# Kernel optimization log

Measured on AMD Instinct MI355X. Metric: run time of the kernel, lower is better.

The kernel has to match this reference:

```python
import jax, jax.numpy as jnp
import numpy as np

B, T, D, H = 4, 2048, 1024, 16
HD = D // H  # head_dim = 64


def setup_inputs() -> dict:
    key = jax.random.key(0)
    ks = jax.random.split(key, 7)
    x = jax.random.normal(ks[0], (B, T, D), dtype=jnp.float32)
    engagement = jax.random.uniform(ks[1], (B, T), dtype=jnp.float32)
    mask = jax.random.uniform(ks[2], (B, T)) < 0.1  # True = masked-out key
    s = 1.0 / np.sqrt(D)
    qkv_w = jax.random.normal(ks[3], (3 * D, D), dtype=jnp.float32) * s
    qkv_b = jax.random.normal(ks[4], (3 * D,), dtype=jnp.float32) * 0.02
    out_w = jax.random.normal(ks[5], (D, D), dtype=jnp.float32) * s
    out_b = jax.random.normal(ks[6], (D,), dtype=jnp.float32) * 0.02
    return {"x": x, "engagement": engagement, "mask": mask,
            "qkv_w": qkv_w, "qkv_b": qkv_b, "out_w": out_w, "out_b": out_b}


def reference(x, engagement, mask, qkv_w, qkv_b, out_w, out_b):
    b, t, d = x.shape
    qkv = x @ qkv_w.T + qkv_b                       # [B,T,3D]
    q, k, v = jnp.split(qkv, 3, axis=-1)
    # [B,T,D] -> [B,H,T,HD]
    to_heads = lambda a: a.reshape(b, t, H, HD).transpose(0, 2, 1, 3)
    q, k, v = to_heads(q), to_heads(k), to_heads(v)
    attn = jnp.einsum('bhqd,bhkd->bhqk', q, k) / jnp.sqrt(jnp.float32(HD))
    log_g = jnp.log(jnp.clip(engagement, 1e-6))     # [B,T] per-key bias
    attn = attn + log_g[:, None, None, :]
    attn = jnp.where(mask[:, None, None, :], jnp.float32(-1e9), attn)
    p = jax.nn.softmax(attn, axis=-1)
    o = jnp.einsum('bhqk,bhkd->bhqd', p, v)         # [B,H,T,HD]
    o = o.transpose(0, 2, 1, 3).reshape(b, t, d)    # [B,T,D]
    return o @ out_w.T + out_b
```

## Files before the change

### kernel.cpp

```cpp
#include <hip/hip_runtime.h>
#include <math.h>

#define B_  4
#define T_  2048
#define D_  1024
#define H_  16
#define HD_ 64

typedef unsigned short ushort_t;
typedef unsigned int uint_t;
typedef __attribute__((ext_vector_type(8))) short bf16x8;
typedef __attribute__((ext_vector_type(4))) float f32x4;

#define SC_LOG2 0.1803368801111243f

__device__ inline ushort_t f2bf(float f) {
  uint_t u = __float_as_uint(f);
  u += 0x7fffu + ((u >> 16) & 1u);
  return (ushort_t)(u >> 16);
}
__device__ inline ushort_t f2bf_fast(float f) {
  return (ushort_t)((__float_as_uint(f) + 0x8000u) >> 16);
}
__device__ inline uint_t cvtpk_bf16(float lo, float hi) {
  uint_t r;
  asm("v_cvt_pk_bf16_f32 %0, %1, %2" : "=v"(r) : "v"(lo), "v"(hi));
  return r;
}

__device__ inline void gload_lds16(const ushort_t* g, ushort_t* l) {
  __builtin_amdgcn_global_load_lds(
      (const __attribute__((address_space(1))) unsigned int*)g,
      (__attribute__((address_space(3))) unsigned int*)l, 16, 0, 0);
}

__global__ __launch_bounds__(256) void cvt_bf16(const float* __restrict__ in,
                                                ushort_t* __restrict__ out, int n) {
  int i = (blockIdx.x * 256 + threadIdx.x) * 4;
  if (i + 3 < n) {
    float4 v = *(const float4*)(in + i);
    uint_t lo = (uint_t)f2bf(v.x) | ((uint_t)f2bf(v.y) << 16);
    uint_t hi = (uint_t)f2bf(v.z) | ((uint_t)f2bf(v.w) << 16);
    *(uint2*)(out + i) = make_uint2(lo, hi);
  }
}

__global__ __launch_bounds__(256) void bias_prep(const float* __restrict__ eng,
                                                 const int* __restrict__ mask,
                                                 float* __restrict__ biasA, int n) {
  int i = blockIdx.x * 256 + threadIdx.x;
  if (i < n) biasA[i] = mask[i] ? -1e30f : __log2f(fmaxf(eng[i], 1e-6f));
}

#define CHUNKS_ 32

#define STAGE_CHUNK(CK, SLOT)                                                  \
  {                                                                            \
    const int ck_ = (CK);                                                      \
    ushort_t* sb_ = lds + (SLOT) * SLOT_E;                                     \
    gload_lds16(Ag + (size_t)ck_ * 32, sb_ + w * 512);                         \
    if constexpr (BN == 256) {                                                 \
      gload_lds16(Bg + (size_t)ck_ * 32, sb_ + 4096 + w * 1024);               \
      gload_lds16(Bg + 16384 + (size_t)ck_ * 32, sb_ + 4096 + w * 1024 + 512); \
    } else {                                                                   \
      gload_lds16(Bg + (size_t)ck_ * 32, sb_ + 4096 + w * 512);                \
    }                                                                          \
  }

template <int WRITE_BF16, int BN>
__global__ __launch_bounds__(512, 4) void gemm256(
    const ushort_t* __restrict__ A, const ushort_t* __restrict__ Bm,
    const float* __restrict__ bias, void* __restrict__ Cout,
    int N, int nbx) {
  constexpr int SLOT_E = 4096 + BN * 32;
  constexpr int NBB = BN / 64;
  constexpr int WCOLS = BN / 4;
  __shared__ __align__(16) ushort_t lds[3 * SLOT_E];

  const int tid = threadIdx.x;
  const int w = tid >> 6, lane = tid & 63;
  const int l15 = lane & 15, quad = lane >> 4;
  const int wr = w >> 2, wc = w & 3;

  int wg = blockIdx.x;
  const int cpx = gridDim.x >> 3;
  wg = (wg & 7) * cpx + (wg >> 3);
  const int m0 = (wg / nbx) * 128, n0 = (wg % nbx) * BN;

  const int gc = (lane & 3) ^ ((lane >> 3) & 3);
  const ushort_t* Ag = A + (size_t)(m0 + w * 16 + (lane >> 2)) * 1024 + gc * 8;
  const ushort_t* Bg =
      Bm + (size_t)(n0 + w * (BN / 8) + (lane >> 2)) * 1024 + gc * 8;

  const int p8 = (quad ^ ((l15 >> 1) & 3)) * 8;
  const int rowA = (wr * 64 + l15) * 32 + p8;
  const int rowB = 4096 + (wc * WCOLS + l15) * 32 + p8;

  f32x4 acc[4][NBB];
#pragma unroll
  for (int mb = 0; mb < 4; ++mb)
#pragma unroll
    for (int nb = 0; nb < NBB; ++nb) acc[mb][nb] = (f32x4){0.f, 0.f, 0.f, 0.f};

  STAGE_CHUNK(0, 0);
  STAGE_CHUNK(1, 1);
  if constexpr (BN == 256)
    asm volatile("s_waitcnt vmcnt(3)" ::: "memory");
  else
    asm volatile("s_waitcnt vmcnt(2)" ::: "memory");
  __builtin_amdgcn_s_barrier();
  __builtin_amdgcn_sched_barrier(0);

  int s_cur = 0;
#pragma unroll 1
  for (int ph = 0; ph < CHUNKS_; ++ph) {
    const ushort_t* Ls = lds + s_cur * SLOT_E;
    bf16x8 af[4], bf[NBB];
#pragma unroll
    for (int mb = 0; mb < 4; ++mb)
      af[mb] = *(const bf16x8*)(Ls + rowA + mb * 512);
#pragma unroll
    for (int nb = 0; nb < NBB; ++nb)
      bf[nb] = *(const bf16x8*)(Ls + rowB + nb * 512);
    if (ph < CHUNKS_ - 2) {
      const int s_n2 = (s_cur == 0) ? 2 : s_cur - 1;
      STAGE_CHUNK(ph + 2, s_n2);
    }
    __builtin_amdgcn_s_setprio(1);
#pragma unroll
    for (int mb = 0; mb < 4; ++mb)
#pragma unroll
      for (int nb = 0; nb < NBB; ++nb)
        acc[mb][nb] = __builtin_amdgcn_mfma_f32_16x16x32_bf16(
            af[mb], bf[nb], acc[mb][nb], 0, 0, 0);
    __builtin_amdgcn_s_setprio(0);
    if (ph < CHUNKS_ - 2) {
      if constexpr (BN == 256)
        asm volatile("s_waitcnt vmcnt(3)" ::: "memory");
      else
        asm volatile("s_waitcnt vmcnt(2)" ::: "memory");
    } else {
      asm volatile("s_waitcnt vmcnt(0)" ::: "memory");
    }
    __builtin_amdgcn_s_barrier();
    __builtin_amdgcn_sched_barrier(0);
    s_cur = (s_cur == 2) ? 0 : s_cur + 1;
  }

  float bb[NBB];
#pragma unroll
  for (int nb = 0; nb < NBB; ++nb)
    bb[nb] = bias[n0 + wc * WCOLS + nb * 16 + l15];

  if constexpr (WRITE_BF16) {
    ushort_t* patch = lds + w * 4608;
    ushort_t* Cb = (ushort_t*)Cout;
#pragma unroll
    for (int mb = 0; mb < 4; ++mb)
#pragma unroll
      for (int nb = 0; nb < NBB; ++nb)
#pragma unroll
        for (int i = 0; i < 4; ++i)
          patch[(mb * 16 + quad * 4 + i) * 72 + nb * 16 + l15] =
              f2bf_fast(acc[mb][nb][i] + bb[nb]);
#pragma unroll
    for (int it = 0; it < 8; ++it) {
      int rl = it * 8 + (lane >> 3);
      size_t grow = (size_t)(m0 + wr * 64 + rl);
      uint4 v = *(const uint4*)&patch[rl * 72 + (lane & 7) * 8];
      *(uint4*)&Cb[grow * N + n0 + wc * WCOLS + (lane & 7) * 8] = v;
    }
  } else {
    float* Cf = (float*)Cout;
#pragma unroll
    for (int mb = 0; mb < 4; ++mb)
#pragma unroll
      for (int i = 0; i < 4; ++i) {
        size_t row = (size_t)(m0 + wr * 64 + mb * 16 + quad * 4 + i);
#pragma unroll
        for (int nb = 0; nb < NBB; ++nb)
          Cf[row * N + n0 + wc * WCOLS + nb * 16 + l15] =
              acc[mb][nb][i] + bb[nb];
      }
  }
}

#define ATTN_TILE(K0, Kc, Vc, bc, Kn, Vn, bn, PF)                              \
  {                                                                            \
    uint4 va_, vc_;                                                            \
    const bool pf_ = (PF);                                                     \
    if (pf_) {                                                                 \
      const int k1_ = (K0) + 64;                                               \
      gload_lds16(kbase + (size_t)(k1_ + w * 8 + kr8) * rs + kgc * 8,          \
                  &(Kn)[(w * 8) * 64]);                                        \
      if (tid < 256) {                                                         \
        const ushort_t* vp_ = vbase + (size_t)(k1_ + 2 * kp) * rs + cc * 8;    \
        va_ = *(const uint4*)vp_;                                              \
        vc_ = *(const uint4*)(vp_ + rs);                                       \
      }                                                                        \
      if (tid < 64) (bn)[tid] = bptr[k1_ + tid];                               \
    }                                                                          \
    bf16x8 kf0[4], kf1[4];                                                     \
    _Pragma("unroll")                                                          \
    for (int nb = 0; nb < 4; ++nb) {                                           \
      int key = nb * 16 + l15;                                                 \
      int p0 = (quad ^ (key & 7)) * 8;                                         \
      kf0[nb] = *(const bf16x8*)(&(Kc)[key * 64 + p0]);                        \
      kf1[nb] = *(const bf16x8*)(&(Kc)[key * 64 + (p0 ^ 32)]);                 \
    }                                                                          \
    bf16x8 vf0[4], vf1[4];                                                     \
    _Pragma("unroll")                                                          \
    for (int nbd = 0; nbd < 4; ++nbd) {                                        \
      vf0[nbd] = *(const bf16x8*)(&(Vc)[quad * 520 + (nbd * 16 + l15) * 8]);   \
      vf1[nbd] =                                                               \
          *(const bf16x8*)(&(Vc)[(4 + quad) * 520 + (nbd * 16 + l15) * 8]);    \
    }                                                                          \
    _Pragma("unroll")                                                          \
    for (int qb = 0; qb < 2; ++qb) {                                           \
      f32x4 st[4];                                                             \
      __builtin_amdgcn_s_setprio(1);                                           \
      _Pragma("unroll")                                                        \
      for (int nb = 0; nb < 4; ++nb) {                                         \
        f32x4 s = (f32x4){0.f, 0.f, 0.f, 0.f};                                 \
        s = __builtin_amdgcn_mfma_f32_16x16x32_bf16(kf0[nb], qf[qb][0], s, 0,  \
                                                    0, 0);                     \
        s = __builtin_amdgcn_mfma_f32_16x16x32_bf16(kf1[nb], qf[qb][1], s, 0,  \
                                                    0, 0);                     \
        st[nb] = s;                                                            \
      }                                                                        \
      __builtin_amdgcn_s_setprio(0);                                           \
      float pp[4][4];                                                          \
      float racc = 0.f;                                                        \
      _Pragma("unroll")                                                        \
      for (int nb = 0; nb < 4; ++nb) {                                         \
        f32x4 bv = *(const f32x4*)&(bc)[nb * 16 + quad * 4];                   \
        _Pragma("unroll")                                                      \
        for (int i = 0; i < 4; ++i) {                                          \
          float p = __builtin_amdgcn_exp2f(st[nb][i] * SC_LOG2 + bv[i]);       \
          pp[nb][i] = p;                                                       \
          racc += p;                                                           \
        }                                                                      \
      }                                                                        \
      rsum[qb] += racc;                                                        \
      union { uint4 u; bf16x8 v; } pf0, pf1;                                   \
      pf0.u.x = cvtpk_bf16(pp[0][0], pp[0][1]);                                \
      pf0.u.y = cvtpk_bf16(pp[0][2], pp[0][3]);                                \
      pf0.u.z = cvtpk_bf16(pp[1][0], pp[1][1]);                                \
      pf0.u.w = cvtpk_bf16(pp[1][2], pp[1][3]);                                \
      pf1.u.x = cvtpk_bf16(pp[2][0], pp[2][1]);                                \
      pf1.u.y = cvtpk_bf16(pp[2][2], pp[2][3]);                                \
      pf1.u.z = cvtpk_bf16(pp[3][0], pp[3][1]);                                \
      pf1.u.w = cvtpk_bf16(pp[3][2], pp[3][3]);                                \
      __builtin_amdgcn_s_setprio(1);                                           \
      _Pragma("unroll")                                                        \
      for (int nbd = 0; nbd < 4; ++nbd) {                                      \
        Oa[qb][nbd] = __builtin_amdgcn_mfma_f32_16x16x32_bf16(                 \
            pf0.v, vf0[nbd], Oa[qb][nbd], 0, 0, 0);                            \
        Oa[qb][nbd] = __builtin_amdgcn_mfma_f32_16x16x32_bf16(                 \
            pf1.v, vf1[nbd], Oa[qb][nbd], 0, 0, 0);                            \
      }                                                                        \
      __builtin_amdgcn_s_setprio(0);                                           \
    }                                                                          \
    if (pf_ && tid < 256) {                                                    \
      uint_t* dst_ = (uint_t*)&(Vn)[gp * 520 + cc * 64 + j0];                  \
      dst_[0]  = (va_.x & 0xffffu) | (vc_.x << 16);                            \
      dst_[4]  = (va_.x >> 16)     | (vc_.x & 0xffff0000u);                    \
      dst_[8]  = (va_.y & 0xffffu) | (vc_.y << 16);                            \
      dst_[12] = (va_.y >> 16)     | (vc_.y & 0xffff0000u);                    \
      dst_[16] = (va_.z & 0xffffu) | (vc_.z << 16);                            \
      dst_[20] = (va_.z >> 16)     | (vc_.z & 0xffff0000u);                    \
      dst_[24] = (va_.w & 0xffffu) | (vc_.w << 16);                            \
      dst_[28] = (va_.w >> 16)     | (vc_.w & 0xffff0000u);                    \
    }                                                                          \
    __syncthreads();                                                           \
  }

__global__ __launch_bounds__(512) void attn_mfma(
    const ushort_t* __restrict__ qkv, const float* __restrict__ biasA,
    ushort_t* __restrict__ oat) {
  __shared__ __align__(16) char smem[37888];
  ushort_t* Kb0 = (ushort_t*)(smem);
  ushort_t* Kb1 = (ushort_t*)(smem + 8192);
  ushort_t* Vb0 = (ushort_t*)(smem + 16384);
  ushort_t* Vb1 = (ushort_t*)(smem + 24704);
  float* bsh0 = (float*)(smem + 33024);
  float* bsh1 = (float*)(smem + 33280);
  float (*lsum)[32] = (float (*)[32])(smem + 36864);

  const int b = blockIdx.z, h = blockIdx.y;
  const int q0 = blockIdx.x * 256;
  const int tid = threadIdx.x;
  const int w = tid >> 6, lane = tid & 63;
  const int l15 = lane & 15, quad = lane >> 4;
  const size_t rs = 3 * D_;

  bf16x8 qf[2][2];
#pragma unroll
  for (int qb = 0; qb < 2; ++qb) {
    const ushort_t* qp =
        qkv + (size_t)(b * T_ + q0 + w * 32 + qb * 16 + l15) * rs + h * HD_;
    qf[qb][0] = *(const bf16x8*)(qp + quad * 8);
    qf[qb][1] = *(const bf16x8*)(qp + 32 + quad * 8);
  }

  f32x4 Oa[2][4];
#pragma unroll
  for (int qb = 0; qb < 2; ++qb)
#pragma unroll
    for (int nb = 0; nb < 4; ++nb) Oa[qb][nb] = (f32x4){0.f, 0.f, 0.f, 0.f};
  float rsum[2] = {0.f, 0.f};

  const ushort_t* kbase = qkv + (size_t)(b * T_) * rs + D_ + h * HD_;
  const ushort_t* vbase = kbase + D_;
  const float* bptr = biasA + b * T_;

  const int kr8 = lane >> 3;
  const int kgc = (lane & 7) ^ kr8;
  const int kp = tid & 31, cc = tid >> 5;
  const int gp = (kp >> 4) * 4 + ((kp >> 1) & 3);
  const int j0 = ((kp >> 3) & 1) * 4 + 2 * (kp & 1);

  {
    gload_lds16(kbase + (size_t)(w * 8 + kr8) * rs + kgc * 8,
                &Kb0[(w * 8) * 64]);
    if (tid < 256) {
      const ushort_t* vp = vbase + (size_t)(2 * kp) * rs + cc * 8;
      uint4 va = *(const uint4*)vp;
      uint4 vc = *(const uint4*)(vp + rs);
      uint_t* dst = (uint_t*)&Vb0[gp * 520 + cc * 64 + j0];
      dst[0]  = (va.x & 0xffffu) | (vc.x << 16);
      dst[4]  = (va.x >> 16)     | (vc.x & 0xffff0000u);
      dst[8]  = (va.y & 0xffffu) | (vc.y << 16);
      dst[12] = (va.y >> 16)     | (vc.y & 0xffff0000u);
      dst[16] = (va.z & 0xffffu) | (vc.z << 16);
      dst[20] = (va.z >> 16)     | (vc.z & 0xffff0000u);
      dst[24] = (va.w & 0xffffu) | (vc.w << 16);
      dst[28] = (va.w >> 16)     | (vc.w & 0xffff0000u);
    }
    if (tid < 64) bsh0[tid] = bptr[tid];
  }
  __syncthreads();

  for (int k0 = 0; k0 < T_; k0 += 128) {
    ATTN_TILE(k0,      Kb0, Vb0, bsh0, Kb1, Vb1, bsh1, true);
    ATTN_TILE(k0 + 64, Kb1, Vb1, bsh1, Kb0, Vb0, bsh0, k0 + 128 < T_);
  }

#pragma unroll
  for (int qb = 0; qb < 2; ++qb) {
    float r = rsum[qb];
    r += __shfl_xor(r, 16, 64);
    r += __shfl_xor(r, 32, 64);
    if (lane < 16) lsum[w][qb * 16 + lane] = r;
  }
  ushort_t* OstW = (ushort_t*)(smem) + w * 2304;
#pragma unroll
  for (int qb = 0; qb < 2; ++qb) {
    f32x4 lr = *(const f32x4*)&lsum[w][qb * 16 + quad * 4];
    f32x4 invl;
#pragma unroll
    for (int i = 0; i < 4; ++i) invl[i] = __builtin_amdgcn_rcpf(lr[i]);
#pragma unroll
    for (int nbd = 0; nbd < 4; ++nbd)
#pragma unroll
      for (int i = 0; i < 4; ++i)
        OstW[(qb * 16 + quad * 4 + i) * 72 + nbd * 16 + l15] =
            f2bf_fast(Oa[qb][nbd][i] * invl[i]);
  }
  ushort_t* dst = oat + (size_t)(b * T_ + q0 + w * 32) * D_ + h * HD_;
#pragma unroll
  for (int pp = 0; pp < 4; ++pp) {
    int row = pp * 8 + (lane >> 3), c = lane & 7;
    uint4 v = *(const uint4*)&OstW[row * 72 + c * 8];
    *(uint4*)&dst[(size_t)row * D_ + c * 8] = v;
  }
}

extern "C" void kernel_launch(void* const* d_in, const int* in_sizes, int n_in,
                              void* d_out, int out_size, void* d_ws, size_t ws_size,
                              hipStream_t stream) {
  const float* x     = (const float*)d_in[0];
  const float* eng   = (const float*)d_in[1];
  const int*   mask  = (const int*)d_in[2];
  const float* qkv_w = (const float*)d_in[3];
  const float* qkv_b = (const float*)d_in[4];
  const float* out_w = (const float*)d_in[5];
  const float* out_b = (const float*)d_in[6];
  float* out = (float*)d_out;

  const int M = B_ * T_;
  const size_t nx = (size_t)M * D_;
  const size_t nwq = (size_t)3 * D_ * D_;
  const size_t nwo = (size_t)D_ * D_;
  const size_t nqkv = (size_t)M * 3 * D_;

  char* p = (char*)d_ws;
  ushort_t* xb    = (ushort_t*)p;            p += nx * 2;
  ushort_t* wqkvb = (ushort_t*)p;            p += nwq * 2;
  ushort_t* woutb = (ushort_t*)p;            p += nwo * 2;
  ushort_t* qkvb  = (ushort_t*)p;            p += nqkv * 2;
  ushort_t* oatb  = (ushort_t*)p;            p += nx * 2;
  float*    biasA = (float*)p;               p += (size_t)M * 4;

  cvt_bf16<<<(int)(nx / 1024), 256, 0, stream>>>(x, xb, (int)nx);
  cvt_bf16<<<(int)(nwq / 1024), 256, 0, stream>>>(qkv_w, wqkvb, (int)nwq);
  cvt_bf16<<<(int)(nwo / 1024), 256, 0, stream>>>(out_w, woutb, (int)nwo);
  bias_prep<<<M / 256, 256, 0, stream>>>(eng, mask, biasA, M);

  gemm256<1, 256><<<768, 512, 0, stream>>>(xb, wqkvb, qkv_b, qkvb, 3 * D_, 12);
  attn_mfma<<<dim3(T_ / 256, H_, B_), 512, 0, stream>>>(qkvb, biasA, oatb);
  gemm256<0, 128><<<512, 512, 0, stream>>>(oatb, woutb, out_b, out, D_, 8);
}
```

Measured before the change: 282.6 us.

## Enlarge GEMM tiles to 256 rows with 1024 threads and double attention key tile

Result: no change. 286.9 us (+1.5%).

```diff
diff --git a/kernel.cpp b/kernel.cpp
--- a/kernel.cpp
+++ b/kernel.cpp
@@ -56,25 +56,21 @@
 
 #define STAGE_CHUNK(CK, SLOT)                                                  \
   {                                                                            \
-    const int ck_ = (CK);                                                      \
     ushort_t* sb_ = lds + (SLOT) * SLOT_E;                                     \
-    gload_lds16(Ag + (size_t)ck_ * 32, sb_ + w * 512);                         \
-    if constexpr (BN == 256) {                                                 \
-      gload_lds16(Bg + (size_t)ck_ * 32, sb_ + 4096 + w * 1024);               \
-      gload_lds16(Bg + 16384 + (size_t)ck_ * 32, sb_ + 4096 + w * 1024 + 512); \
-    } else {                                                                   \
-      gload_lds16(Bg + (size_t)ck_ * 32, sb_ + 4096 + w * 512);                \
-    }                                                                          \
+    gload_lds16(Ag + (size_t)(CK) * 32, sb_ + w * 512);                        \
+    if (BN == 256 || w < 8)                                                    \
+      gload_lds16(Bg + (size_t)(CK) * 32, sb_ + 8192 + w * 512);               \
   }
 
 template <int WRITE_BF16, int BN>
-__global__ __launch_bounds__(512, 4) void gemm256(
+__global__ __launch_bounds__(1024) void gemm256(
     const ushort_t* __restrict__ A, const ushort_t* __restrict__ Bm,
     const float* __restrict__ bias, void* __restrict__ Cout,
     int N, int nbx) {
-  constexpr int SLOT_E = 4096 + BN * 32;
+  constexpr int SLOT_E = 8192 + BN * 32;
   constexpr int NBB = BN / 64;
   constexpr int WCOLS = BN / 4;
+  constexpr int WAITC = (BN == 256) ? 2 : 1;
   __shared__ __align__(16) ushort_t lds[3 * SLOT_E];
 
   const int tid = threadIdx.x;
@@ -85,16 +81,16 @@
   int wg = blockIdx.x;
   const int cpx = gridDim.x >> 3;
   wg = (wg & 7) * cpx + (wg >> 3);
-  const int m0 = (wg / nbx) * 128, n0 = (wg % nbx) * BN;
+  const int m0 = (wg / nbx) * 256, n0 = (wg % nbx) * BN;
 
   const int gc = (lane & 3) ^ ((lane >> 3) & 3);
   const ushort_t* Ag = A + (size_t)(m0 + w * 16 + (lane >> 2)) * 1024 + gc * 8;
   const ushort_t* Bg =
-      Bm + (size_t)(n0 + w * (BN / 8) + (lane >> 2)) * 1024 + gc * 8;
+      Bm + (size_t)(n0 + w * 16 + (lane >> 2)) * 1024 + gc * 8;
 
   const int p8 = (quad ^ ((l15 >> 1) & 3)) * 8;
   const int rowA = (wr * 64 + l15) * 32 + p8;
-  const int rowB = 4096 + (wc * WCOLS + l15) * 32 + p8;
+  const int rowB = 8192 + (wc * WCOLS + l15) * 32 + p8;
 
   f32x4 acc[4][NBB];
 #pragma unroll
@@ -104,10 +100,7 @@
 
   STAGE_CHUNK(0, 0);
   STAGE_CHUNK(1, 1);
-  if constexpr (BN == 256)
-    asm volatile("s_waitcnt vmcnt(3)" ::: "memory");
-  else
-    asm volatile("s_waitcnt vmcnt(2)" ::: "memory");
+  asm volatile("s_waitcnt vmcnt(%0)" :: "i"(WAITC) : "memory");
   __builtin_amdgcn_s_barrier();
   __builtin_amdgcn_sched_barrier(0);
 
@@ -134,14 +127,10 @@
         acc[mb][nb] = __builtin_amdgcn_mfma_f32_16x16x32_bf16(
             af[mb], bf[nb], acc[mb][nb], 0, 0, 0);
     __builtin_amdgcn_s_setprio(0);
-    if (ph < CHUNKS_ - 2) {
-      if constexpr (BN == 256)
-        asm volatile("s_waitcnt vmcnt(3)" ::: "memory");
-      else
-        asm volatile("s_waitcnt vmcnt(2)" ::: "memory");
-    } else {
+    if (ph < CHUNKS_ - 2)
+      asm volatile("s_waitcnt vmcnt(%0)" :: "i"(WAITC) : "memory");
+    else
       asm volatile("s_waitcnt vmcnt(0)" ::: "memory");
-    }
     __builtin_amdgcn_s_barrier();
     __builtin_amdgcn_sched_barrier(0);
     s_cur = (s_cur == 2) ? 0 : s_cur + 1;
@@ -153,22 +142,27 @@
     bb[nb] = bias[n0 + wc * WCOLS + nb * 16 + l15];
 
   if constexpr (WRITE_BF16) {
-    ushort_t* patch = lds + w * 4608;
+    ushort_t* patch = lds + w * 2304;
     ushort_t* Cb = (ushort_t*)Cout;
 #pragma unroll
-    for (int mb = 0; mb < 4; ++mb)
-#pragma unroll
-      for (int nb = 0; nb < NBB; ++nb)
-#pragma unroll
-        for (int i = 0; i < 4; ++i)
-          patch[(mb * 16 + quad * 4 + i) * 72 + nb * 16 + l15] =
-              f2bf_fast(acc[mb][nb][i] + bb[nb]);
-#pragma unroll
-    for (int it = 0; it < 8; ++it) {
-      int rl = it * 8 + (lane >> 3);
-      size_t grow = (size_t)(m0 + wr * 64 + rl);
-      uint4 v = *(const uint4*)&patch[rl * 72 + (lane & 7) * 8];
-      *(uint4*)&Cb[grow * N + n0 + wc * WCOLS + (lane & 7) * 8] = v;
+    for (int half = 0; half < 2; ++half) {
+#pragma unroll
+      for (int mb2 = 0; mb2 < 2; ++mb2) {
+        const int mb = half * 2 + mb2;
+#pragma unroll
+        for (int nb = 0; nb < NBB; ++nb)
+#pragma unroll
+          for (int i = 0; i < 4; ++i)
+            patch[(mb2 * 16 + quad * 4 + i) * 72 + nb * 16 + l15] =
+                f2bf_fast(acc[mb][nb][i] + bb[nb]);
+      }
+#pragma unroll
+      for (int it = 0; it < 4; ++it) {
+        int rl = it * 8 + (lane >> 3);
+        size_t grow = (size_t)(m0 + wr * 64 + half * 32 + rl);
+        uint4 v = *(const uint4*)&patch[rl * 72 + (lane & 7) * 8];
+        *(uint4*)&Cb[grow * N + n0 + wc * WCOLS + (lane & 7) * 8] = v;
+      }
     }
   } else {
     float* Cf = (float*)Cout;
@@ -190,79 +184,86 @@
     uint4 va_, vc_;                                                            \
     const bool pf_ = (PF);                                                     \
     if (pf_) {                                                                 \
-      const int k1_ = (K0) + 64;                                               \
-      gload_lds16(kbase + (size_t)(k1_ + w * 8 + kr8) * rs + kgc * 8,          \
-                  &(Kn)[(w * 8) * 64]);                                        \
-      if (tid < 256) {                                                         \
-        const ushort_t* vp_ = vbase + (size_t)(k1_ + 2 * kp) * rs + cc * 8;    \
+      const int k1_ = (K0) + 128;                                              \
+      _Pragma("unroll")                                                        \
+      for (int u = 0; u < 2; ++u)                                              \
+        gload_lds16(kbase + (size_t)(k1_ + w * 16 + u * 8 + kr8) * rs + kgc * 8,\
+                    &(Kn)[(w * 16 + u * 8) * 64]);                             \
+      {                                                                        \
+        const ushort_t* vp_ = vbase + (size_t)(k1_ + vkey) * rs + cc * 8;      \
         va_ = *(const uint4*)vp_;                                              \
         vc_ = *(const uint4*)(vp_ + rs);                                       \
       }                                                                        \
-      if (tid < 64) (bn)[tid] = bptr[k1_ + tid];                               \
-    }                                                                          \
-    bf16x8 kf0[4], kf1[4];                                                     \
-    _Pragma("unroll")                                                          \
-    for (int nb = 0; nb < 4; ++nb) {                                           \
-      int key = nb * 16 + l15;                                                 \
-      int p0 = (quad ^ (key & 7)) * 8;                                         \
-      kf0[nb] = *(const bf16x8*)(&(Kc)[key * 64 + p0]);                        \
-      kf1[nb] = *(const bf16x8*)(&(Kc)[key * 64 + (p0 ^ 32)]);                 \
-    }                                                                          \
-    bf16x8 vf0[4], vf1[4];                                                     \
-    _Pragma("unroll")                                                          \
-    for (int nbd = 0; nbd < 4; ++nbd) {                                        \
-      vf0[nbd] = *(const bf16x8*)(&(Vc)[quad * 520 + (nbd * 16 + l15) * 8]);   \
-      vf1[nbd] =                                                               \
-          *(const bf16x8*)(&(Vc)[(4 + quad) * 520 + (nbd * 16 + l15) * 8]);    \
+      if (tid < 128) (bn)[tid] = bptr[k1_ + tid];                              \
     }                                                                          \
     _Pragma("unroll")                                                          \
-    for (int qb = 0; qb < 2; ++qb) {                                           \
-      f32x4 st[4];                                                             \
-      __builtin_amdgcn_s_setprio(1);                                           \
+    for (int ks = 0; ks < 2; ++ks) {                                           \
+      const ushort_t* Kcs = (Kc) + ks * 4096;                                  \
+      const ushort_t* Vcs = (Vc) + ks * 4160;                                  \
+      const float* bcs = (bc) + ks * 64;                                       \
+      bf16x8 kf0[4], kf1[4];                                                   \
       _Pragma("unroll")                                                        \
       for (int nb = 0; nb < 4; ++nb) {                                         \
-        f32x4 s = (f32x4){0.f, 0.f, 0.f, 0.f};                                 \
-        s = __builtin_amdgcn_mfma_f32_16x16x32_bf16(kf0[nb], qf[qb][0], s, 0,  \
-                                                    0, 0);                     \
-        s = __builtin_amdgcn_mfma_f32_16x16x32_bf16(kf1[nb], qf[qb][1], s, 0,  \
-                                                    0, 0);                     \
-        st[nb] = s;                                                            \
+        int key = nb * 16 + l15;                                               \
+        int p0 = (quad ^ (key & 7)) * 8;                                       \
+        kf0[nb] = *(const bf16x8*)(&Kcs[key * 64 + p0]);                       \
+        kf1[nb] = *(const bf16x8*)(&Kcs[key * 64 + (p0 ^ 32)]);                \
       }                                                                        \
-      __builtin_amdgcn_s_setprio(0);                                           \
-      float pp[4][4];                                                          \
-      float racc = 0.f;                                                        \
-      _Pragma("unroll")                                                        \
-      for (int nb = 0; nb < 4; ++nb) {                                         \
-        f32x4 bv = *(const f32x4*)&(bc)[nb * 16 + quad * 4];                   \
-        _Pragma("unroll")                                                      \
-        for (int i = 0; i < 4; ++i) {                                          \
-          float p = __builtin_amdgcn_exp2f(st[nb][i] * SC_LOG2 + bv[i]);       \
-          pp[nb][i] = p;                                                       \
-          racc += p;                                                           \
-        }                                                                      \
-      }                                                                        \
-      rsum[qb] += racc;                                                        \
-      union { uint4 u; bf16x8 v; } pf0, pf1;                                   \
-      pf0.u.x = cvtpk_bf16(pp[0][0], pp[0][1]);                                \
-      pf0.u.y = cvtpk_bf16(pp[0][2], pp[0][3]);                                \
-      pf0.u.z = cvtpk_bf16(pp[1][0], pp[1][1]);                                \
-      pf0.u.w = cvtpk_bf16(pp[1][2], pp[1][3]);                                \
-      pf1.u.x = cvtpk_bf16(pp[2][0], pp[2][1]);                                \
-      pf1.u.y = cvtpk_bf16(pp[2][2], pp[2][3]);                                \
-      pf1.u.z = cvtpk_bf16(pp[3][0], pp[3][1]);                                \
-      pf1.u.w = cvtpk_bf16(pp[3][2], pp[3][3]);                                \
-      __builtin_amdgcn_s_setprio(1);                                           \
+      bf16x8 vf0[4], vf1[4];                                                   \
       _Pragma("unroll")                                                        \
       for (int nbd = 0; nbd < 4; ++nbd) {                                      \
-        Oa[qb][nbd] = __builtin_amdgcn_mfma_f32_16x16x32_bf16(                 \
-            pf0.v, vf0[nbd], Oa[qb][nbd], 0, 0, 0);                            \
-        Oa[qb][nbd] = __builtin_amdgcn_mfma_f32_16x16x32_bf16(                 \
-            pf1.v, vf1[nbd], Oa[qb][nbd], 0, 0, 0);                            \
+        vf0[nbd] = *(const bf16x8*)(&Vcs[quad * 520 + (nbd * 16 + l15) * 8]);  \
+        vf1[nbd] =                                                             \
+            *(const bf16x8*)(&Vcs[(4 + quad) * 520 + (nbd * 16 + l15) * 8]);   \
       }                                                                        \
-      __builtin_amdgcn_s_setprio(0);                                           \
+      _Pragma("unroll")                                                        \
+      for (int qb = 0; qb < 2; ++qb) {                                         \
+        f32x4 st[4];                                                           \
+        __builtin_amdgcn_s_setprio(1);                                         \
+        _Pragma("unroll")                                                      \
+        for (int nb = 0; nb < 4; ++nb) {                                       \
+          f32x4 s = (f32x4){0.f, 0.f, 0.f, 0.f};                               \
+          s = __builtin_amdgcn_mfma_f32_16x16x32_bf16(kf0[nb], qf[qb][0], s,   \
+                                                      0, 0, 0);                \
+          s = __builtin_amdgcn_mfma_f32_16x16x32_bf16(kf1[nb], qf[qb][1], s,   \
+                                                      0, 0, 0);                \
+          st[nb] = s;                                                          \
+        }                                                                      \
+        __builtin_amdgcn_s_setprio(0);                                         \
+        float pp[4][4];                                                        \
+        _Pragma("unroll")                                                      \
+        for (int nb = 0; nb < 4; ++nb) {                                       \
+          f32x4 bv = *(const f32x4*)&bcs[nb * 16 + quad * 4];                  \
+          _Pragma("unroll")                                                    \
+          for (int i = 0; i < 4; ++i)                                          \
+            pp[nb][i] = __builtin_amdgcn_exp2f(st[nb][i] * SC_LOG2 + bv[i]);   \
+        }                                                                      \
+        union { uint4 u; bf16x8 v; } pf0, pf1;                                 \
+        pf0.u.x = cvtpk_bf16(pp[0][0], pp[0][1]);                              \
+        pf0.u.y = cvtpk_bf16(pp[0][2], pp[0][3]);                              \
+        pf0.u.z = cvtpk_bf16(pp[1][0], pp[1][1]);                              \
+        pf0.u.w = cvtpk_bf16(pp[1][2], pp[1][3]);                              \
+        pf1.u.x = cvtpk_bf16(pp[2][0], pp[2][1]);                              \
+        pf1.u.y = cvtpk_bf16(pp[2][2], pp[2][3]);                              \
+        pf1.u.z = cvtpk_bf16(pp[3][0], pp[3][1]);                              \
+        pf1.u.w = cvtpk_bf16(pp[3][2], pp[3][3]);                              \
+        __builtin_amdgcn_s_setprio(1);                                         \
+        _Pragma("unroll")                                                      \
+        for (int nbd = 0; nbd < 4; ++nbd) {                                    \
+          Oa[qb][nbd] = __builtin_amdgcn_mfma_f32_16x16x32_bf16(               \
+              pf0.v, vf0[nbd], Oa[qb][nbd], 0, 0, 0);                          \
+          Oa[qb][nbd] = __builtin_amdgcn_mfma_f32_16x16x32_bf16(               \
+              pf1.v, vf1[nbd], Oa[qb][nbd], 0, 0, 0);                          \
+        }                                                                      \
+        Osum[qb] = __builtin_amdgcn_mfma_f32_16x16x32_bf16(                    \
+            pf0.v, onesf.v, Osum[qb], 0, 0, 0);                                \
+        Osum[qb] = __builtin_amdgcn_mfma_f32_16x16x32_bf16(                    \
+            pf1.v, onesf.v, Osum[qb], 0, 0, 0);                                \
+        __builtin_amdgcn_s_setprio(0);                                         \
+      }                                                                        \
     }                                                                          \
-    if (pf_ && tid < 256) {                                                    \
-      uint_t* dst_ = (uint_t*)&(Vn)[gp * 520 + cc * 64 + j0];                  \
+    if (pf_) {                                                                 \
+      uint_t* dst_ = (uint_t*)&(Vn)[vs * 4160 + gp * 520 + cc * 64 + j0];      \
       dst_[0]  = (va_.x & 0xffffu) | (vc_.x << 16);                            \
       dst_[4]  = (va_.x >> 16)     | (vc_.x & 0xffff0000u);                    \
       dst_[8]  = (va_.y & 0xffffu) | (vc_.y << 16);                            \
@@ -278,14 +279,13 @@
 __global__ __launch_bounds__(512) void attn_mfma(
     const ushort_t* __restrict__ qkv, const float* __restrict__ biasA,
     ushort_t* __restrict__ oat) {
-  __shared__ __align__(16) char smem[37888];
+  __shared__ __align__(16) char smem[67072];
   ushort_t* Kb0 = (ushort_t*)(smem);
-  ushort_t* Kb1 = (ushort_t*)(smem + 8192);
-  ushort_t* Vb0 = (ushort_t*)(smem + 16384);
-  ushort_t* Vb1 = (ushort_t*)(smem + 24704);
-  float* bsh0 = (float*)(smem + 33024);
-  float* bsh1 = (float*)(smem + 33280);
-  float (*lsum)[32] = (float (*)[32])(smem + 36864);
+  ushort_t* Kb1 = (ushort_t*)(smem + 16384);
+  ushort_t* Vb0 = (ushort_t*)(smem + 32768);
+  ushort_t* Vb1 = (ushort_t*)(smem + 49408);
+  float* bsh0 = (float*)(smem + 66048);
+  float* bsh1 = (float*)(smem + 66560);
 
   const int b = blockIdx.z, h = blockIdx.y;
   const int q0 = blockIdx.x * 256;
@@ -303,12 +303,15 @@
     qf[qb][1] = *(const bf16x8*)(qp + 32 + quad * 8);
   }
 
-  f32x4 Oa[2][4];
-#pragma unroll
-  for (int qb = 0; qb < 2; ++qb)
+  f32x4 Oa[2][4], Osum[2];
+#pragma unroll
+  for (int qb = 0; qb < 2; ++qb) {
+    Osum[qb] = (f32x4){0.f, 0.f, 0.f, 0.f};
 #pragma unroll
     for (int nb = 0; nb < 4; ++nb) Oa[qb][nb] = (f32x4){0.f, 0.f, 0.f, 0.f};
-  float rsum[2] = {0.f, 0.f};
+  }
+  union { uint4 u; bf16x8 v; } onesf;
+  onesf.u = make_uint4(0x3F803F80u, 0x3F803F80u, 0x3F803F80u, 0x3F803F80u);
 
   const ushort_t* kbase = qkv + (size_t)(b * T_) * rs + D_ + h * HD_;
   const ushort_t* vbase = kbase + D_;
@@ -316,50 +319,44 @@
 
   const int kr8 = lane >> 3;
   const int kgc = (lane & 7) ^ kr8;
-  const int kp = tid & 31, cc = tid >> 5;
+  const int vs = tid >> 8, tv = tid & 255;
+  const int kp = tv & 31, cc = tv >> 5;
+  const int vkey = vs * 64 + 2 * kp;
   const int gp = (kp >> 4) * 4 + ((kp >> 1) & 3);
   const int j0 = ((kp >> 3) & 1) * 4 + 2 * (kp & 1);
 
   {
-    gload_lds16(kbase + (size_t)(w * 8 + kr8) * rs + kgc * 8,
-                &Kb0[(w * 8) * 64]);
-    if (tid < 256) {
-      const ushort_t* vp = vbase + (size_t)(2 * kp) * rs + cc * 8;
-      uint4 va = *(const uint4*)vp;
-      uint4 vc = *(const uint4*)(vp + rs);
-      uint_t* dst = (uint_t*)&Vb0[gp * 520 + cc * 64 + j0];
-      dst[0]  = (va.x & 0xffffu) | (vc.x << 16);
-      dst[4]  = (va.x >> 16)     | (vc.x & 0xffff0000u);
-      dst[8]  = (va.y & 0xffffu) | (vc.y << 16);
-      dst[12] = (va.y >> 16)     | (vc.y & 0xffff0000u);
-      dst[16] = (va.z & 0xffffu) | (vc.z << 16);
-      dst[20] = (va.z >> 16)     | (vc.z & 0xffff0000u);
-      dst[24] = (va.w & 0xffffu) | (vc.w << 16);
-      dst[28] = (va.w >> 16)     | (vc.w & 0xffff0000u);
-    }
-    if (tid < 64) bsh0[tid] = bptr[tid];
+#pragma unroll
+    for (int u = 0; u < 2; ++u)
+      gload_lds16(kbase + (size_t)(w * 16 + u * 8 + kr8) * rs + kgc * 8,
+                  &Kb0[(w * 16 + u * 8) * 64]);
+    const ushort_t* vp = vbase + (size_t)vkey * rs + cc * 8;
+    uint4 va = *(const uint4*)vp;
+    uint4 vc = *(const uint4*)(vp + rs);
+    uint_t* dst = (uint_t*)&Vb0[vs * 4160 + gp * 520 + cc * 64 + j0];
+    dst[0]  = (va.x & 0xffffu) | (vc.x << 16);
+    dst[4]  = (va.x >> 16)     | (vc.x & 0xffff0000u);
+    dst[8]  = (va.y & 0xffffu) | (vc.y << 16);
+    dst[12] = (va.y >> 16)     | (vc.y & 0xffff0000u);
+    dst[16] = (va.z & 0xffffu) | (vc.z << 16);
+    dst[20] = (va.z >> 16)     | (vc.z & 0xffff0000u);
+    dst[24] = (va.w & 0xffffu) | (vc.w << 16);
+    dst[28] = (va.w >> 16)     | (vc.w & 0xffff0000u);
+    if (tid < 128) bsh0[tid] = bptr[tid];
   }
   __syncthreads();
 
-  for (int k0 = 0; k0 < T_; k0 += 128) {
-    ATTN_TILE(k0,      Kb0, Vb0, bsh0, Kb1, Vb1, bsh1, true);
-    ATTN_TILE(k0 + 64, Kb1, Vb1, bsh1, Kb0, Vb0, bsh0, k0 + 128 < T_);
-  }
-
+  for (int k0 = 0; k0 < T_; k0 += 256) {
+    ATTN_TILE(k0,       Kb0, Vb0, bsh0, Kb1, Vb1, bsh1, true);
+    ATTN_TILE(k0 + 128, Kb1, Vb1, bsh1, Kb0, Vb0, bsh0, k0 + 256 < T_);
+  }
+
+  ushort_t* OstW = (ushort_t*)(smem) + w * 2304;
 #pragma unroll
   for (int qb = 0; qb < 2; ++qb) {
-    float r = rsum[qb];
-    r += __shfl_xor(r, 16, 64);
-    r += __shfl_xor(r, 32, 64);
-    if (lane < 16) lsum[w][qb * 16 + lane] = r;
-  }
-  ushort_t* OstW = (ushort_t*)(smem) + w * 2304;
-#pragma unroll
-  for (int qb = 0; qb < 2; ++qb) {
-    f32x4 lr = *(const f32x4*)&lsum[w][qb * 16 + quad * 4];
     f32x4 invl;
 #pragma unroll
-    for (int i = 0; i < 4; ++i) invl[i] = __builtin_amdgcn_rcpf(lr[i]);
+    for (int i = 0; i < 4; ++i) invl[i] = __builtin_amdgcn_rcpf(Osum[qb][i]);
 #pragma unroll
     for (int nbd = 0; nbd < 4; ++nbd)
 #pragma unroll
@@ -407,7 +404,7 @@
   cvt_bf16<<<(int)(nwo / 1024), 256, 0, stream>>>(out_w, woutb, (int)nwo);
   bias_prep<<<M / 256, 256, 0, stream>>>(eng, mask, biasA, M);
 
-  gemm256<1, 256><<<768, 512, 0, stream>>>(xb, wqkvb, qkv_b, qkvb, 3 * D_, 12);
+  gemm256<1, 256><<<384, 1024, 0, stream>>>(xb, wqkvb, qkv_b, qkvb, 3 * D_, 12);
   attn_mfma<<<dim3(T_ / 256, H_, B_), 512, 0, stream>>>(qkvb, biasA, oatb);
-  gemm256<0, 128><<<512, 512, 0, stream>>>(oatb, woutb, out_b, out, D_, 8);
-}
+  gemm256<0, 128><<<256, 1024, 0, stream>>>(oatb, woutb, out_b, out, D_, 8);
+}
```
